# Optimization experiments

Hardware: AMD Instinct MI355X
Metric: run time of the kernel (lower is better)

The kernel has to match this reference:

```python
import jax, jax.numpy as jnp
import numpy as np

DELTA = 6.0      # 3 / (1 - alpha), alpha = 0.5
ETA = 1.0
MS_ITER = 3
D_FEAT = 256
N_PTS = 8192
X_SCALE = 0.06   # keeps ||x||^2 ~ 0.9 so exp(DELTA * X^T X) is well-conditioned


def setup_inputs() -> dict:
    key = jax.random.key(0)
    X = jax.random.normal(key, (D_FEAT, N_PTS), dtype=jnp.float32) * X_SCALE
    return {"X": X}


def _mean_shift_once(X):
    # X: [d, N]
    S = jnp.einsum('dn,dm->nm', X, X)          # X^T X, [N, N]
    K = jnp.exp(DELTA * S)                     # Gaussian-like affinity, [N, N]
    colsum = jnp.sum(K, axis=0)                # d = K^T @ ones  -> column sums, [N]
    # X @ P with P = (1-eta) I + eta K D_inv; D_inv = diag(1/colsum).
    # X @ K @ D_inv == (X @ K) / colsum (per-column scaling) -- no diag/eye materialized.
    XK = X @ K                                 # [d, N]
    return (1.0 - ETA) * X + ETA * (XK / colsum[None, :])


def reference(X):
    outs = []
    cur = X
    for _ in range(MS_ITER):
        cur = _mean_shift_once(cur)
        outs.append(cur)
    return tuple(outs)
```

## Files before the change

### kernel.cpp

```cpp
#include <hip/hip_runtime.h>
#include <hip/hip_bf16.h>
#include <stdint.h>

#define DFEAT 256
#define NPTS  8192

typedef __attribute__((ext_vector_type(8)))  short bf16x8;
typedef __attribute__((ext_vector_type(16))) float f32x16;
typedef __attribute__((ext_vector_type(4)))  int   int4v;
typedef __attribute__((ext_vector_type(4)))  float f32x4;

#define AS1 __attribute__((address_space(1)))
#define AS3 __attribute__((address_space(3)))

__device__ inline void dma16(const void* g, void* l) {
  __builtin_amdgcn_global_load_lds((const AS1 uint32_t*)g, (AS3 uint32_t*)l, 16, 0, 0);
}

__device__ inline uint16_t f2bf(float f) {
  union { float f; uint32_t u; } v; v.f = f;
  return (uint16_t)((v.u + 0x7FFFu + ((v.u >> 16) & 1u)) >> 16);
}


__global__ __launch_bounds__(256, 2) void ms_fused(
    const uint16_t* __restrict__ xaf,
    const uint16_t* __restrict__ xbf,
    float* __restrict__ num,
    float* __restrict__ cs)
{
  __shared__ __attribute__((aligned(16))) uint16_t XT[2][16384];
  __shared__ __attribute__((aligned(16))) uint16_t Ps[64 * 64];

  const int tid  = threadIdx.x;
  const int w    = tid >> 6;
  const int lane = tid & 63;
  const int l31  = lane & 31;
  const int g    = lane >> 5;
  const int bid  = blockIdx.x;
  const int mt   = (bid & 1) | ((bid >> 3) << 1);
  const int q    = (bid >> 1) & 3;
  const int m0   = mt * 64;
  const int a_sub = w >> 1;
  const int b_sub = w & 1;

  const char* xafc = (const char*)xaf;
  const char* xbfc = (const char*)xbf;
  char*       Psc  = (char*)Ps;

  bf16x8 Bm[16];
  {
    const char* bp = xafc + (size_t)(m0 / 32 + b_sub) * 16384 + g * 512 + l31 * 16;
    #pragma unroll
    for (int ks = 0; ks < 16; ++ks)
      Bm[ks] = __builtin_bit_cast(bf16x8, *(const int4v*)(bp + ks * 1024));
  }

  f32x16 accO[2][2];
  #pragma unroll
  for (int i = 0; i < 2; ++i)
    #pragma unroll
    for (int j = 0; j < 2; ++j)
      #pragma unroll
      for (int r = 0; r < 16; ++r) accO[i][j][r] = 0.0f;
  float csacc = 0.0f;

  const int mloc = 32 * b_sub + l31;
  const int l7   = l31 & 7;
  const int j0   = q * 32;

  {
    const char* src = xafc + (size_t)j0 * 32768;
    #pragma unroll
    for (int r = 0; r < 8; ++r)
      dma16(src + tid * 16 + r * 4096, (char*)XT[0] + tid * 16 + r * 4096);
  }

  for (int t = 0; t < 32; ++t) {
    const int jt  = j0 + t;
    const int cur = t & 1;
    __syncthreads();

    if (t < 31) {
      const char* src = xafc + (size_t)(jt + 1) * 32768;
      #pragma unroll
      for (int r = 0; r < 8; ++r)
        dma16(src + tid * 16 + r * 4096,
              (char*)XT[cur ^ 1] + tid * 16 + r * 4096);
    }

    const int n0 = jt * 64;
    bf16x8 Xf[2][4];
    #pragma unroll
    for (int t2 = 0; t2 < 2; ++t2) {
      const char* xp = xbfc + (size_t)(2 * w + t2) * 524288 +
                       (size_t)(n0 >> 3) * 512 + g * 512 + l31 * 16;
      #pragma unroll
      for (int ks = 0; ks < 4; ++ks)
        Xf[t2][ks] = __builtin_bit_cast(bf16x8, *(const int4v*)(xp + ks * 1024));
    }

    f32x16 s;
    #pragma unroll
    for (int r = 0; r < 16; ++r) s[r] = 0.0f;
    {
      const char* ap = (const char*)XT[cur] + a_sub * 16384 + g * 512 + l31 * 16;
      #pragma unroll
      for (int ks = 0; ks < 16; ++ks) {
        bf16x8 A = __builtin_bit_cast(bf16x8, *(const int4v*)(ap + ks * 1024));
        s = __builtin_amdgcn_mfma_f32_32x32x16_bf16(A, Bm[ks], s, 0, 0, 0);
      }
    }

    #pragma unroll
    for (int k = 0; k < 4; ++k) {
      float e0 = __expf(6.0f * s[4*k+0]);
      float e1 = __expf(6.0f * s[4*k+1]);
      float e2 = __expf(6.0f * s[4*k+2]);
      float e3 = __expf(6.0f * s[4*k+3]);
      csacc += (e0 + e1) + (e2 + e3);
      uint32_t lo, hi;
      asm("v_cvt_pk_bf16_f32 %0, %1, %2" : "=v"(lo) : "v"(e0), "v"(e1));
      asm("v_cvt_pk_bf16_f32 %0, %1, %2" : "=v"(hi) : "v"(e2), "v"(e3));
      int p = (4 * a_sub + k) ^ (mloc & 7);
      *(uint64_t*)(Psc + mloc * 128 + p * 16 + 8 * g) =
          ((uint64_t)hi << 32) | lo;
    }
    __syncthreads();

    #pragma unroll
    for (int ks = 0; ks < 4; ++ks) {
      bf16x8 Bp[2];
      #pragma unroll
      for (int mm = 0; mm < 2; ++mm) {
        int mrow = 32 * mm + l31;
        int p = (2 * ks + g) ^ l7;
        Bp[mm] = __builtin_bit_cast(bf16x8,
            *(const int4v*)(Psc + mrow * 128 + p * 16));
      }
      #pragma unroll
      for (int t2 = 0; t2 < 2; ++t2) {
        accO[t2][0] = __builtin_amdgcn_mfma_f32_32x32x16_bf16(Xf[t2][ks], Bp[0], accO[t2][0], 0,0,0);
        accO[t2][1] = __builtin_amdgcn_mfma_f32_32x32x16_bf16(Xf[t2][ks], Bp[1], accO[t2][1], 0,0,0);
      }
    }
  }

  csacc += __shfl_xor(csacc, 32, 64);
  if (g == 0) atomicAdd(&cs[m0 + mloc], csacc);
  #pragma unroll
  for (int t2 = 0; t2 < 2; ++t2)
    #pragma unroll
    for (int mm = 0; mm < 2; ++mm)
      #pragma unroll
      for (int r = 0; r < 16; ++r) {
        int drow = 32 * (2 * w + t2) + (r & 3) + 8 * (r >> 2) + 4 * g;
        int mg   = m0 + 32 * mm + l31;
        atomicAdd(&num[(size_t)drow * NPTS + mg], accO[t2][mm][r]);
      }
}

__global__ __launch_bounds__(256) void ms_combine(
    const float* __restrict__ src, const float* __restrict__ csr,
    float* __restrict__ csz, float* __restrict__ yout,
    float* __restrict__ numz,
    uint16_t* __restrict__ xaf, uint16_t* __restrict__ xbf,
    const int mode)
{
  __shared__ uint16_t T[64][66];
  const int tid = threadIdx.x;
  const int n0 = blockIdx.x * 64;
  const int d0 = blockIdx.y * 64;

  #pragma unroll
  for (int i = 0; i < 4; ++i) {
    int e  = tid + i * 256;
    int dl = e >> 4, nq = e & 15;
    size_t idx = (size_t)(d0 + dl) * NPTS + (n0 + nq * 4);
    f32x4 v = *(const f32x4*)(src + idx);
    if (mode) {
      f32x4 c = *(const f32x4*)(csr + n0 + nq * 4);
      v /= c;
      *(f32x4*)(yout + idx) = v;
      f32x4 z = {0.f, 0.f, 0.f, 0.f};
      *(f32x4*)(numz + idx) = z;
    }
    #pragma unroll
    for (int k = 0; k < 4; ++k) T[dl][nq * 4 + k] = f2bf(v[k]);
  }
  if (mode && blockIdx.y == 0 && tid < 64) csz[n0 + tid] = 0.0f;
  __syncthreads();

  char* xafc = (char*)xaf;
  char* xbfc = (char*)xbf;
  #pragma unroll
  for (int i = 0; i < 2; ++i) {
    int c  = tid + i * 256;
    int nb = c >> 8, s2 = (c >> 5) & 7, ln = c & 31;
    union { uint32_t u[4]; int4v v; } pk;
    #pragma unroll
    for (int k = 0; k < 4; ++k) {
      uint32_t lo = T[s2 * 8 + 2 * k][nb * 32 + ln];
      uint32_t hi = T[s2 * 8 + 2 * k + 1][nb * 32 + ln];
      pk.u[k] = lo | (hi << 16);
    }
    *(int4v*)(xafc + (size_t)(n0 / 32 + nb) * 16384 +
              (size_t)(d0 / 8 + s2) * 512 + ln * 16) = pk.v;
  }
  #pragma unroll
  for (int i = 0; i < 2; ++i) {
    int c  = tid + i * 256;
    int db = c >> 8, uu = (c >> 5) & 7, ln = c & 31;
    const uint16_t* tr = &T[db * 32 + ln][uu * 8];
    union { uint32_t u[4]; int4v v; } pk;
    #pragma unroll
    for (int k = 0; k < 4; ++k)
      pk.u[k] = (uint32_t)tr[2 * k] | ((uint32_t)tr[2 * k + 1] << 16);
    *(int4v*)(xbfc + (size_t)(d0 / 32 + db) * 524288 +
              (size_t)(n0 / 8 + uu) * 512 + ln * 16) = pk.v;
  }
}

extern "C" void kernel_launch(void* const* d_in, const int* in_sizes, int n_in,
                              void* d_out, int out_size, void* d_ws, size_t ws_size,
                              hipStream_t stream)
{
  (void)in_sizes; (void)n_in; (void)out_size; (void)ws_size;
  const float* X = (const float*)d_in[0];
  float* out = (float*)d_out;
  char* ws = (char*)d_ws;
  uint16_t* xaf = (uint16_t*)(ws);
  uint16_t* xbf = (uint16_t*)(ws + (4u << 20));
  float*    num = (float*)   (ws + (8u << 20));
  float*    cs0 = (float*)   (ws + (16u << 20));
  float*    cs1 = (float*)   (ws + (16u << 20) + 32768);

  hipMemsetAsync(ws + (8u << 20), 0, (8u << 20) + 65536, stream);

  dim3 cgrid(NPTS / 64, DFEAT / 64);
  ms_combine<<<cgrid, 256, 0, stream>>>(X, nullptr, nullptr, nullptr, nullptr,
                                        xaf, xbf, 0);
  for (int it = 0; it < 3; ++it) {
    float* csA = (it & 1) ? cs1 : cs0;
    float* csB = (it & 1) ? cs0 : cs1;
    ms_fused<<<512, 256, 0, stream>>>(xaf, xbf, num, csA);
    ms_combine<<<cgrid, 256, 0, stream>>>(num, csA, csB,
                                          out + (size_t)it * DFEAT * NPTS,
                                          num, xaf, xbf, 1);
  }
}
```

Before: 351.5 us.

## Software-pipeline fused mean-shift loop with double-buffered P tile and single barrier

Double-buffers the exp-affinity tile in LDS so the X·P accumulation for the previous tile runs in the same iteration as the S = XᵀX MFMA chain for the current tile. This cuts one __syncthreads per iteration and moves the next-tile DMA and the Xf global loads later, to overlap them with compute. A manual s_waitcnt vmcnt(8) plus a raw s_barrier replaces the full sync, and a drain step handles the last tile after the loop. The LDS footprint grows by 8KB, and correctness now depends on the hand-tuned wait counts.

```diff
diff --git a/kernel.cpp b/kernel.cpp
--- a/kernel.cpp
+++ b/kernel.cpp
@@ -30,7 +30,7 @@
     float* __restrict__ cs)
 {
   __shared__ __attribute__((aligned(16))) uint16_t XT[2][16384];
-  __shared__ __attribute__((aligned(16))) uint16_t Ps[64 * 64];
+  __shared__ __attribute__((aligned(16))) uint16_t Ps[2][4096];
 
   const int tid  = threadIdx.x;
   const int w    = tid >> 6;
@@ -46,6 +46,7 @@
 
   const char* xafc = (const char*)xaf;
   const char* xbfc = (const char*)xbf;
+  char*       XTc  = (char*)XT;
   char*       Psc  = (char*)Ps;
 
   bf16x8 Bm[16];
@@ -73,42 +74,67 @@
     const char* src = xafc + (size_t)j0 * 32768;
     #pragma unroll
     for (int r = 0; r < 8; ++r)
-      dma16(src + tid * 16 + r * 4096, (char*)XT[0] + tid * 16 + r * 4096);
-  }
+      dma16(src + tid * 16 + r * 4096, XTc + tid * 16 + r * 4096);
+  }
+  __syncthreads();
+
+  bf16x8 Xf[2][4];
 
   for (int t = 0; t < 32; ++t) {
     const int jt  = j0 + t;
     const int cur = t & 1;
-    __syncthreads();
-
-    if (t < 31) {
-      const char* src = xafc + (size_t)(jt + 1) * 32768;
-      #pragma unroll
-      for (int r = 0; r < 8; ++r)
-        dma16(src + tid * 16 + r * 4096,
-              (char*)XT[cur ^ 1] + tid * 16 + r * 4096);
-    }
-
-    const int n0 = jt * 64;
-    bf16x8 Xf[2][4];
-    #pragma unroll
-    for (int t2 = 0; t2 < 2; ++t2) {
-      const char* xp = xbfc + (size_t)(2 * w + t2) * 524288 +
-                       (size_t)(n0 >> 3) * 512 + g * 512 + l31 * 16;
-      #pragma unroll
-      for (int ks = 0; ks < 4; ++ks)
-        Xf[t2][ks] = __builtin_bit_cast(bf16x8, *(const int4v*)(xp + ks * 1024));
-    }
+    char*       psW = Psc + cur * 8192;
+    const char* psR = Psc + (cur ^ 1) * 8192;
 
     f32x16 s;
     #pragma unroll
     for (int r = 0; r < 16; ++r) s[r] = 0.0f;
     {
-      const char* ap = (const char*)XT[cur] + a_sub * 16384 + g * 512 + l31 * 16;
+      const char* ap = XTc + cur * 32768 + a_sub * 16384 + g * 512 + l31 * 16;
       #pragma unroll
       for (int ks = 0; ks < 16; ++ks) {
         bf16x8 A = __builtin_bit_cast(bf16x8, *(const int4v*)(ap + ks * 1024));
         s = __builtin_amdgcn_mfma_f32_32x32x16_bf16(A, Bm[ks], s, 0, 0, 0);
+      }
+    }
+
+    if (t < 31) {
+      const char* src = xafc + (size_t)(jt + 1) * 32768;
+      #pragma unroll
+      for (int r = 0; r < 8; ++r)
+        dma16(src + tid * 16 + r * 4096,
+              XTc + (cur ^ 1) * 32768 + tid * 16 + r * 4096);
+    }
+    __builtin_amdgcn_sched_barrier(0x38F);
+
+    if (t > 0) {
+      #pragma unroll
+      for (int ks = 0; ks < 4; ++ks) {
+        bf16x8 Bp[2];
+        #pragma unroll
+        for (int mm = 0; mm < 2; ++mm) {
+          int mrow = 32 * mm + l31;
+          int p = (2 * ks + g) ^ l7;
+          Bp[mm] = __builtin_bit_cast(bf16x8,
+              *(const int4v*)(psR + mrow * 128 + p * 16));
+        }
+        #pragma unroll
+        for (int t2 = 0; t2 < 2; ++t2) {
+          accO[t2][0] = __builtin_amdgcn_mfma_f32_32x32x16_bf16(Xf[t2][ks], Bp[0], accO[t2][0], 0,0,0);
+          accO[t2][1] = __builtin_amdgcn_mfma_f32_32x32x16_bf16(Xf[t2][ks], Bp[1], accO[t2][1], 0,0,0);
+        }
+      }
+    }
+
+    {
+      const int n0 = jt * 64;
+      #pragma unroll
+      for (int t2 = 0; t2 < 2; ++t2) {
+        const char* xp = xbfc + (size_t)(2 * w + t2) * 524288 +
+                         (size_t)(n0 >> 3) * 512 + g * 512 + l31 * 16;
+        #pragma unroll
+        for (int ks = 0; ks < 4; ++ks)
+          Xf[t2][ks] = __builtin_bit_cast(bf16x8, *(const int4v*)(xp + ks * 1024));
       }
     }
 
@@ -123,11 +149,16 @@
       asm("v_cvt_pk_bf16_f32 %0, %1, %2" : "=v"(lo) : "v"(e0), "v"(e1));
       asm("v_cvt_pk_bf16_f32 %0, %1, %2" : "=v"(hi) : "v"(e2), "v"(e3));
       int p = (4 * a_sub + k) ^ (mloc & 7);
-      *(uint64_t*)(Psc + mloc * 128 + p * 16 + 8 * g) =
+      *(uint64_t*)(psW + mloc * 128 + p * 16 + 8 * g) =
           ((uint64_t)hi << 32) | lo;
     }
-    __syncthreads();
-
+
+    asm volatile("s_waitcnt vmcnt(8) lgkmcnt(0)" ::: "memory");
+    __builtin_amdgcn_s_barrier();
+  }
+
+  {
+    const char* psR = Psc + 8192;
     #pragma unroll
     for (int ks = 0; ks < 4; ++ks) {
       bf16x8 Bp[2];
@@ -136,7 +167,7 @@
         int mrow = 32 * mm + l31;
         int p = (2 * ks + g) ^ l7;
         Bp[mm] = __builtin_bit_cast(bf16x8,
-            *(const int4v*)(Psc + mrow * 128 + p * 16));
+            *(const int4v*)(psR + mrow * 128 + p * 16));
       }
       #pragma unroll
       for (int t2 = 0; t2 < 2; ++t2) {
```

After: 338.1 us. -3.8%, faster.

## Software-pipeline PV matmul one tile behind QK with double-buffered P

Applied to the files above, without the earlier changes.

Restructures the fused loop so that the P·X accumulation for tile t-1 is issued alongside the S computation and exp for tile t. P gets a double buffer in LDS, and the X fragments for the B side alternate between two register sets. The two barriers per tile become one, using an explicit waitcnt that leaves the next XT DMA in flight. This aims to overlap exp/VALU work with MFMA and cut synchronisation, at the cost of more registers and LDS, which may reduce occupancy below 2 blocks per CU.

```diff
diff --git a/kernel.cpp b/kernel.cpp
--- a/kernel.cpp
+++ b/kernel.cpp
@@ -30,7 +30,7 @@
     float* __restrict__ cs)
 {
   __shared__ __attribute__((aligned(16))) uint16_t XT[2][16384];
-  __shared__ __attribute__((aligned(16))) uint16_t Ps[64 * 64];
+  __shared__ __attribute__((aligned(16))) uint16_t Ps[2][4096];
 
   const int tid  = threadIdx.x;
   const int w    = tid >> 6;
@@ -46,6 +46,7 @@
 
   const char* xafc = (const char*)xaf;
   const char* xbfc = (const char*)xbf;
+  char*       XTc  = (char*)XT;
   char*       Psc  = (char*)Ps;
 
   bf16x8 Bm[16];
@@ -73,61 +74,106 @@
     const char* src = xafc + (size_t)j0 * 32768;
     #pragma unroll
     for (int r = 0; r < 8; ++r)
-      dma16(src + tid * 16 + r * 4096, (char*)XT[0] + tid * 16 + r * 4096);
-  }
-
-  for (int t = 0; t < 32; ++t) {
-    const int jt  = j0 + t;
-    const int cur = t & 1;
-    __syncthreads();
-
-    if (t < 31) {
-      const char* src = xafc + (size_t)(jt + 1) * 32768;
-      #pragma unroll
-      for (int r = 0; r < 8; ++r)
-        dma16(src + tid * 16 + r * 4096,
-              (char*)XT[cur ^ 1] + tid * 16 + r * 4096);
-    }
-
-    const int n0 = jt * 64;
-    bf16x8 Xf[2][4];
-    #pragma unroll
-    for (int t2 = 0; t2 < 2; ++t2) {
-      const char* xp = xbfc + (size_t)(2 * w + t2) * 524288 +
-                       (size_t)(n0 >> 3) * 512 + g * 512 + l31 * 16;
-      #pragma unroll
-      for (int ks = 0; ks < 4; ++ks)
-        Xf[t2][ks] = __builtin_bit_cast(bf16x8, *(const int4v*)(xp + ks * 1024));
-    }
-
-    f32x16 s;
-    #pragma unroll
-    for (int r = 0; r < 16; ++r) s[r] = 0.0f;
-    {
-      const char* ap = (const char*)XT[cur] + a_sub * 16384 + g * 512 + l31 * 16;
-      #pragma unroll
-      for (int ks = 0; ks < 16; ++ks) {
-        bf16x8 A = __builtin_bit_cast(bf16x8, *(const int4v*)(ap + ks * 1024));
-        s = __builtin_amdgcn_mfma_f32_32x32x16_bf16(A, Bm[ks], s, 0, 0, 0);
-      }
-    }
-
-    #pragma unroll
-    for (int k = 0; k < 4; ++k) {
-      float e0 = __expf(6.0f * s[4*k+0]);
-      float e1 = __expf(6.0f * s[4*k+1]);
-      float e2 = __expf(6.0f * s[4*k+2]);
-      float e3 = __expf(6.0f * s[4*k+3]);
-      csacc += (e0 + e1) + (e2 + e3);
-      uint32_t lo, hi;
-      asm("v_cvt_pk_bf16_f32 %0, %1, %2" : "=v"(lo) : "v"(e0), "v"(e1));
-      asm("v_cvt_pk_bf16_f32 %0, %1, %2" : "=v"(hi) : "v"(e2), "v"(e3));
-      int p = (4 * a_sub + k) ^ (mloc & 7);
-      *(uint64_t*)(Psc + mloc * 128 + p * 16 + 8 * g) =
-          ((uint64_t)hi << 32) | lo;
-    }
-    __syncthreads();
-
+      dma16(src + tid * 16 + r * 4096, XTc + tid * 16 + r * 4096);
+  }
+  __syncthreads();
+
+  bf16x8 XfE[2][4], XfO[2][4];
+
+#define MS_BODY(T_, CUR_, XF_LD, XF_USE, DO_PV)                               \
+  {                                                                           \
+    const int jt_ = j0 + (T_);                                                \
+    char*       psW_ = Psc + (CUR_) * 8192;                                   \
+    const char* psR_ = Psc + ((CUR_) ^ 1) * 8192;                             \
+                         \
+    if ((T_) < 31) {                                                          \
+      const char* src_ = xafc + (size_t)(jt_ + 1) * 32768;                    \
+      _Pragma("unroll")                                                       \
+      for (int r = 0; r < 8; ++r)                                             \
+        dma16(src_ + tid * 16 + r * 4096,                                     \
+              XTc + ((CUR_) ^ 1) * 32768 + tid * 16 + r * 4096);              \
+    }                                                                         \
+                                \
+    {                                                                         \
+      const int n0_ = jt_ * 64;                                               \
+      _Pragma("unroll")                                                       \
+      for (int t2 = 0; t2 < 2; ++t2) {                                        \
+        const char* xp_ = xbfc + (size_t)(2 * w + t2) * 524288 +              \
+                          (size_t)(n0_ >> 3) * 512 + g * 512 + l31 * 16;      \
+        _Pragma("unroll")                                                     \
+        for (int ks = 0; ks < 4; ++ks)                                        \
+          XF_LD[t2][ks] =                                                     \
+              __builtin_bit_cast(bf16x8, *(const int4v*)(xp_ + ks * 1024));   \
+      }                                                                       \
+    }                                                                         \
+              \
+    __builtin_amdgcn_sched_barrier(0x38F);                                    \
+              \
+    f32x16 s;                                                                 \
+    _Pragma("unroll")                                                         \
+    for (int r = 0; r < 16; ++r) s[r] = 0.0f;                                 \
+    {                                                                         \
+      const char* ap_ = XTc + (CUR_) * 32768 + a_sub * 16384 + g * 512 +      \
+                        l31 * 16;                                             \
+      _Pragma("unroll")                                                       \
+      for (int ks = 0; ks < 16; ++ks) {                                       \
+        bf16x8 A = __builtin_bit_cast(bf16x8,                                 \
+                                      *(const int4v*)(ap_ + ks * 1024));      \
+        s = __builtin_amdgcn_mfma_f32_32x32x16_bf16(A, Bm[ks], s, 0, 0, 0);   \
+      }                                                                       \
+    }                                                                         \
+                                \
+    if (DO_PV) {                                                              \
+      _Pragma("unroll")                                                       \
+      for (int ks = 0; ks < 4; ++ks) {                                        \
+        bf16x8 Bp[2];                                                         \
+        _Pragma("unroll")                                                     \
+        for (int mm = 0; mm < 2; ++mm) {                                      \
+          int mrow = 32 * mm + l31;                                           \
+          int p = (2 * ks + g) ^ l7;                                          \
+          Bp[mm] = __builtin_bit_cast(bf16x8,                                 \
+              *(const int4v*)(psR_ + mrow * 128 + p * 16));                   \
+        }                                                                     \
+        _Pragma("unroll")                                                     \
+        for (int t2 = 0; t2 < 2; ++t2) {                                      \
+          accO[t2][0] = __builtin_amdgcn_mfma_f32_32x32x16_bf16(              \
+              XF_USE[t2][ks], Bp[0], accO[t2][0], 0, 0, 0);                   \
+          accO[t2][1] = __builtin_amdgcn_mfma_f32_32x32x16_bf16(              \
+              XF_USE[t2][ks], Bp[1], accO[t2][1], 0, 0, 0);                   \
+        }                                                                     \
+      }                                                                       \
+    }                                                                         \
+                        \
+    _Pragma("unroll")                                                         \
+    for (int k = 0; k < 4; ++k) {                                             \
+      float e0 = __expf(6.0f * s[4 * k + 0]);                                 \
+      float e1 = __expf(6.0f * s[4 * k + 1]);                                 \
+      float e2 = __expf(6.0f * s[4 * k + 2]);                                 \
+      float e3 = __expf(6.0f * s[4 * k + 3]);                                 \
+      csacc += (e0 + e1) + (e2 + e3);                                         \
+      uint32_t lo, hi;                                                        \
+      asm("v_cvt_pk_bf16_f32 %0, %1, %2" : "=v"(lo) : "v"(e0), "v"(e1));      \
+      asm("v_cvt_pk_bf16_f32 %0, %1, %2" : "=v"(hi) : "v"(e2), "v"(e3));      \
+      int p = (4 * a_sub + k) ^ (mloc & 7);                                   \
+      *(uint64_t*)(psW_ + mloc * 128 + p * 16 + 8 * g) =                      \
+          ((uint64_t)hi << 32) | lo;                                          \
+    }                                                                         \
+          \
+    asm volatile("s_waitcnt vmcnt(8) lgkmcnt(0)" ::: "memory");               \
+    __builtin_amdgcn_s_barrier();                                             \
+  }
+
+  MS_BODY(0, 0, XfE, XfO, false)
+  for (int tp = 0; tp < 15; ++tp) {
+    const int tb = 2 * tp;
+    MS_BODY(tb + 1, 1, XfO, XfE, true)
+    MS_BODY(tb + 2, 0, XfE, XfO, true)
+  }
+  MS_BODY(31, 1, XfO, XfE, true)
+#undef MS_BODY
+
+  {
+    const char* psR = Psc + 8192;
     #pragma unroll
     for (int ks = 0; ks < 4; ++ks) {
       bf16x8 Bp[2];
@@ -136,12 +182,12 @@
         int mrow = 32 * mm + l31;
         int p = (2 * ks + g) ^ l7;
         Bp[mm] = __builtin_bit_cast(bf16x8,
-            *(const int4v*)(Psc + mrow * 128 + p * 16));
+            *(const int4v*)(psR + mrow * 128 + p * 16));
       }
       #pragma unroll
       for (int t2 = 0; t2 < 2; ++t2) {
-        accO[t2][0] = __builtin_amdgcn_mfma_f32_32x32x16_bf16(Xf[t2][ks], Bp[0], accO[t2][0], 0,0,0);
-        accO[t2][1] = __builtin_amdgcn_mfma_f32_32x32x16_bf16(Xf[t2][ks], Bp[1], accO[t2][1], 0,0,0);
+        accO[t2][0] = __builtin_amdgcn_mfma_f32_32x32x16_bf16(XfO[t2][ks], Bp[0], accO[t2][0], 0,0,0);
+        accO[t2][1] = __builtin_amdgcn_mfma_f32_32x32x16_bf16(XfO[t2][ks], Bp[1], accO[t2][1], 0,0,0);
       }
     }
   }
```

After: 337.5 us. 4.0% less time.
